# Kernel tuning notes

Hardware: AMD Instinct MI355X
Metric: run time of the kernel (lower is better)

## Reference

```python
import jax, jax.numpy as jnp
import numpy as np

# Static configuration (mirrors init_kwargs)
B, C, H, W = 4, 256, 128, 128
S, T = 512, 64          # style_dim, num style tokens
HC, HS = 4, 8           # cross-attn heads, spatial-attn heads
WS, G = 8, 4            # window size, groupnorm groups
SHARPEN = 2.0
EPS = 1e-5


def _ln(x, g, b):
    m = jnp.mean(x, -1, keepdims=True)
    v = jnp.var(x, -1, keepdims=True)
    return (x - m) * jax.lax.rsqrt(v + EPS) * g + b


def _sdpa(q, k, v, scale):
    # q,k,v: [B, nH, L, D]
    s = jnp.einsum('bhqd,bhkd->bhqk', q, k) * scale
    return jnp.einsum('bhqk,bhkd->bhqd', jax.nn.softmax(s, -1), v)


def _heads(t, nh):
    b, l, c = t.shape
    return t.reshape(b, l, nh, c // nh).transpose(0, 2, 1, 3)


def _unheads(t):
    b, nh, l, d = t.shape
    return t.transpose(0, 2, 1, 3).reshape(b, l, nh * d)


def setup_inputs() -> dict:
    key = jax.random.key(0)
    ks = iter(jax.random.split(key, 48))
    def w(shape, s=0.02):
        return jax.random.normal(next(ks), shape, jnp.float32) * s
    return {
        'x': jax.random.normal(next(ks), (B, C, H, W), jnp.float32),
        'style_code': jax.random.normal(next(ks), (B, S), jnp.float32),
        # SpatialSelfAttention params (1x1 convs == linear over channels)
        'qkv_w': w((3 * C, C)), 'spat_proj_w': w((C, C)),
        # CrossAttnAdaGN params
        'gproj_w': w((2 * C, S)),
        'gproj_b': jnp.concatenate([jnp.ones((C,), jnp.float32), jnp.zeros((C,), jnp.float32)]),
        'tokens_basis': w((T, C)),
        'sproj_w': w((C, S)), 'sproj_b': jnp.zeros((C,), jnp.float32),
        'pos_w1': w((C, 2)), 'pos_b1': jnp.zeros((C,), jnp.float32),
        'pos_w2': w((C, C)), 'pos_b2': jnp.zeros((C,), jnp.float32),
        'q_w': w((C, C)), 'q_b': jnp.zeros((C,), jnp.float32),
        'k_w': w((C, C)), 'k_b': jnp.zeros((C,), jnp.float32),
        'v_w': w((C, C)), 'v_b': jnp.zeros((C,), jnp.float32),
        'o_w': w((C, C)), 'o_b': jnp.zeros((C,), jnp.float32),
        'ffn_w1': w((2 * C, C)), 'ffn_b1': jnp.zeros((2 * C,), jnp.float32),
        'ffn_w2': w((C, 2 * C)), 'ffn_b2': jnp.zeros((C,), jnp.float32),
        'tn_g': jnp.ones((C,), jnp.float32), 'tn_b': jnp.zeros((C,), jnp.float32),
        'qn_g': jnp.ones((C,), jnp.float32), 'qn_b': jnp.zeros((C,), jnp.float32),
        'fn_g': jnp.ones((C,), jnp.float32), 'fn_b': jnp.zeros((C,), jnp.float32),
        'gamma': w((1, C, 1, 1), 0.1),
    }


def reference(x, style_code, qkv_w, spat_proj_w, gproj_w, gproj_b, tokens_basis,
              sproj_w, sproj_b, pos_w1, pos_b1, pos_w2, pos_b2,
              q_w, q_b, k_w, k_b, v_w, v_b, o_w, o_b,
              ffn_w1, ffn_b1, ffn_w2, ffn_b2,
              tn_g, tn_b, qn_g, qn_b, fn_g, fn_b, gamma):
    b = x.shape[0]
    hw = H * W
    # ---------- CrossAttnAdaGN style modulation ----------
    xg = x.reshape(b, G, C // G, H, W)
    mu = jnp.mean(xg, (2, 3, 4), keepdims=True)
    var = jnp.var(xg, (2, 3, 4), keepdims=True)
    normalized = ((xg - mu) * jax.lax.rsqrt(var + EPS)).reshape(b, C, H, W)
    gp = style_code @ gproj_w.T + gproj_b           # [B, 2C]
    scale = gp[:, :C, None, None]
    shift = gp[:, C:, None, None]
    style_tokens = tokens_basis[None] + (style_code @ sproj_w.T + sproj_b)[:, None]  # [B,T,C]
    style_tokens = _ln(style_tokens, tn_g, tn_b)
    gy = jnp.linspace(-1.0, 1.0, H)
    gx = jnp.linspace(-1.0, 1.0, W)
    grid_y, grid_x = jnp.meshgrid(gy, gx, indexing='ij')
    pos = jnp.stack([grid_x, grid_y], -1).reshape(hw, 2)                 # [HW,2]
    pos_emb = jax.nn.silu(pos @ pos_w1.T + pos_b1) @ pos_w2.T + pos_b2   # [HW,C]
    tok = normalized.transpose(0, 2, 3, 1).reshape(b, hw, C)
    q_in = _ln(tok + pos_emb[None], qn_g, qn_b)
    q = _heads(q_in @ q_w.T + q_b, HC)                 # [B,HC,HW,hd]
    k = _heads(style_tokens @ k_w.T + k_b, HC)         # [B,HC,T,hd]
    v = _heads(style_tokens @ v_w.T + v_b, HC)
    hd = C // HC
    sc = _unheads(_sdpa(q, k, v, SHARPEN / jnp.sqrt(jnp.float32(hd))))   # [B,HW,C]
    sc = sc @ o_w.T + o_b
    sc = sc + jax.nn.silu(_ln(sc, fn_g, fn_b) @ ffn_w1.T + ffn_b1) @ ffn_w2.T + ffn_b2
    sc_sp = sc.transpose(0, 2, 1).reshape(b, C, H, W)
    adagn = normalized * scale + shift + sc_sp * gamma
    h = x + adagn  # gate = 1.0, residual style modulation
    # ---------- shifted-window self-attention ----------
    sh = WS // 2
    xr = jnp.roll(h, (-sh, -sh), (2, 3))
    qkv = jnp.einsum('oi,bihw->bohw', qkv_w, xr)
    qs, ks_, vs = jnp.split(qkv, 3, axis=1)
    def win(t):  # [B,C,H,W] -> [B*nWin, WS*WS, C]
        return t.reshape(b, C, H // WS, WS, W // WS, WS).transpose(0, 2, 4, 3, 5, 1).reshape(-1, WS * WS, C)
    hd2 = C // HS
    qh = _heads(win(qs), HS)
    kh = _heads(win(ks_), HS)
    vh = _heads(win(vs), HS)
    out = _unheads(_sdpa(qh, kh, vh, 1.0 / jnp.sqrt(jnp.float32(hd2))))
    out = out.reshape(b, H // WS, W // WS, WS, WS, C).transpose(0, 5, 1, 3, 2, 4).reshape(b, C, H, W)
    out = jnp.roll(out, (sh, sh), (2, 3))
    out = jnp.einsum('oi,bihw->bohw', spat_proj_w, out)
    return h + out
```

## Files before the change

kernel.cpp:

```cpp
#include <hip/hip_runtime.h>
#include <stdint.h>

#define DEV __device__ __forceinline__

typedef unsigned short u16;
typedef unsigned int u32;
typedef __attribute__((ext_vector_type(8))) __bf16 bf16x8;
typedef __attribute__((ext_vector_type(4))) float f32x4;

DEV u16 f2b(float f) {
  u32 u = __float_as_uint(f);
  u32 r = (u + 0x7FFFu + ((u >> 16) & 1u)) >> 16;
  return (u16)r;
}
DEV float b2f(u16 u) { return __uint_as_float(((u32)u) << 16); }
DEV void up2(u32 u, float& a, float& b) {
  a = __uint_as_float(u << 16);
  b = __uint_as_float(u & 0xffff0000u);
}
DEV void up8(uint4 t, float* d) {
  up2(t.x, d[0], d[1]); up2(t.y, d[2], d[3]);
  up2(t.z, d[4], d[5]); up2(t.w, d[6], d[7]);
}
DEV float silu_f(float v) { return v / (1.0f + __expf(-v)); }

DEV float redmax16(float v) {
  v = fmaxf(v, __shfl_xor(v, 1));
  v = fmaxf(v, __shfl_xor(v, 2));
  v = fmaxf(v, __shfl_xor(v, 4));
  v = fmaxf(v, __shfl_xor(v, 8));
  return v;
}
DEV float redsum16(float v) {
  v += __shfl_xor(v, 1);
  v += __shfl_xor(v, 2);
  v += __shfl_xor(v, 4);
  v += __shfl_xor(v, 8);
  return v;
}

DEV void gload16(const u16* g, u16* l) {
  __builtin_amdgcn_global_load_lds(
      (const __attribute__((address_space(1))) uint32_t*)(g),
      (__attribute__((address_space(3))) uint32_t*)(l), 16, 0, 0);
}

struct WConv {
  const float* s0; const float* s1; const float* s2; const float* s3;
  const float* s4; const float* s5; const float* s6;
  u16* d0; u16* d1; u16* d2; u16* d3; u16* d4; u16* d5; u16* d6;
};
__global__ void k_conv_all(WConv wc) {
  int i = blockIdx.x * 256 + threadIdx.x;
  if (i >= 180224) return;
  const float* sp[7] = {wc.s0, wc.s1, wc.s2, wc.s3, wc.s4, wc.s5, wc.s6};
  u16* dp[7] = {wc.d0, wc.d1, wc.d2, wc.d3, wc.d4, wc.d5, wc.d6};
  const int n4[7] = {16384, 16384, 32768, 32768, 49152, 16384, 16384};
  int rem = i, seg = 0;
#pragma unroll
  for (int s = 0; s < 7; ++s) {
    if (rem < n4[s]) { seg = s; break; }
    rem -= n4[s];
  }
  float4 v = ((const float4*)sp[seg])[rem];
  u16 t[4] = {f2b(v.x), f2b(v.y), f2b(v.z), f2b(v.w)};
  *(uint2*)(dp[seg] + (rem << 2)) = *(uint2*)t;
}

DEV void breduce2(float& a, float& b, float* red, int tid) {
#pragma unroll
  for (int off = 32; off > 0; off >>= 1) {
    a += __shfl_down(a, off);
    b += __shfl_down(b, off);
  }
  int lane = tid & 63, wv = tid >> 6;
  if (lane == 0) { red[wv * 2] = a; red[wv * 2 + 1] = b; }
  __syncthreads();
  a = red[0] + red[2] + red[4] + red[6];
  b = red[1] + red[3] + red[5] + red[7];
}

template <int XB>
__global__ void k_gn_partial(const float* __restrict__ x, float* __restrict__ partials,
                             u16* __restrict__ xb) {
  __shared__ float red[8];
  int chunk = blockIdx.x;
  size_t base4 = ((size_t)chunk) << 12;
  const float4* x4 = (const float4*)x;
  float a = 0.f, b = 0.f;
#pragma unroll 4
  for (int i = 0; i < 16; ++i) {
    size_t idx = base4 + (i << 8) + threadIdx.x;
    float4 v = x4[idx];
    a += v.x + v.y + v.z + v.w;
    b += v.x * v.x + v.y * v.y + v.z * v.z + v.w * v.w;
    if (XB) {
      u16 t[4] = {f2b(v.x), f2b(v.y), f2b(v.z), f2b(v.w)};
      *(uint2*)(xb + (idx << 2)) = *(uint2*)t;
    }
  }
  breduce2(a, b, red, threadIdx.x);
  if (threadIdx.x == 0) { partials[chunk * 2] = a; partials[chunk * 2 + 1] = b; }
}

__global__ void k_gn_final(const float* __restrict__ partials, float* __restrict__ stats) {
  int g = blockIdx.x, lane = threadIdx.x;
  float a = partials[(((g << 6) + lane) << 1)];
  float b = partials[(((g << 6) + lane) << 1) + 1];
#pragma unroll
  for (int off = 32; off > 0; off >>= 1) {
    a += __shfl_down(a, off);
    b += __shfl_down(b, off);
  }
  if (lane == 0) {
    float mean = a * (1.f / 1048576.f);
    float var = b * (1.f / 1048576.f) - mean * mean;
    stats[g << 1] = mean;
    stats[(g << 1) + 1] = rsqrtf(var + 1e-5f);
  }
}

__global__ void k_style(const float* __restrict__ sc, const float* __restrict__ gw,
                        const float* __restrict__ gb, const float* __restrict__ sw,
                        const float* __restrict__ sb, float* __restrict__ gp,
                        float* __restrict__ stok) {
  __shared__ float row[512];
  int b = blockIdx.y, part = blockIdx.x, tid = threadIdx.x;
  row[tid] = sc[(b << 9) + tid];
  row[tid + 256] = sc[(b << 9) + tid + 256];
  __syncthreads();
  if (part < 2) {
    int o = (part << 8) + tid;
    float s = gb[o];
    const float* wr = gw + ((size_t)o << 9);
#pragma unroll 8
    for (int j = 0; j < 512; ++j) s += row[j] * wr[j];
    gp[(b << 9) + o] = s;
  } else {
    float s = sb[tid];
    const float* wr = sw + ((size_t)tid << 9);
#pragma unroll 8
    for (int j = 0; j < 512; ++j) s += row[j] * wr[j];
    stok[(b << 8) + tid] = s;
  }
}

__global__ void k_styk(const float* __restrict__ tb, const float* __restrict__ stok,
                       const float* __restrict__ g, const float* __restrict__ bt,
                       float* __restrict__ styk) {
  __shared__ float red[8];
  int r = blockIdx.x;
  int b = r >> 6, t = r & 63;
  int c = threadIdx.x;
  float v = tb[(t << 8) + c] + stok[(b << 8) + c];
  float a = v, bb = v * v;
  breduce2(a, bb, red, c);
  float mean = a * (1.f / 256.f);
  float var = bb * (1.f / 256.f) - mean * mean;
  float rs = rsqrtf(var + 1e-5f);
  styk[((size_t)r << 8) + c] = (v - mean) * rs * g[c] + bt[c];
}

__global__ void k_kv(const float* __restrict__ styk, const float* __restrict__ kw,
                     const float* __restrict__ kb, const float* __restrict__ vw,
                     const float* __restrict__ vb, u16* __restrict__ kmat,
                     u16* __restrict__ vmat) {
  __shared__ float srow[256];
  int r = blockIdx.x, c = threadIdx.x;
  srow[c] = styk[((size_t)r << 8) + c];
  __syncthreads();
  float sk = kb[c], sv = vb[c];
  const float* kr = kw + ((size_t)c << 8);
  const float* vr = vw + ((size_t)c << 8);
#pragma unroll 8
  for (int j = 0; j < 256; ++j) { sk += srow[j] * kr[j]; sv += srow[j] * vr[j]; }
  kmat[((size_t)r << 8) + c] = f2b(sk);
  vmat[((size_t)r << 8) + c] = f2b(sv);
}

__global__ void k_posh(const float* __restrict__ w1, const float* __restrict__ b1,
                       u16* __restrict__ posh) {
  int i = blockIdx.x * 256 + threadIdx.x;
  int stride = gridDim.x * 256;
  for (; i < 16384 * 256; i += stride) {
    int p = i >> 8, c = i & 255;
    int y = p >> 7, x = p & 127;
    float gx = -1.f + 2.f * (float)x / 127.f;
    float gy = -1.f + 2.f * (float)y / 127.f;
    float v = gx * w1[c << 1] + gy * w1[(c << 1) + 1] + b1[c];
    posh[i] = f2b(silu_f(v));
  }
}

template <int ACT, int BIAS, int RES, int SPLIT>
__global__ __launch_bounds__(256, 2) void k_gemm2(
    const u16* __restrict__ A, const u16* __restrict__ Bw,
    const float* __restrict__ bias, const u16* __restrict__ res,
    u16* __restrict__ o0, u16* __restrict__ o1, u16* __restrict__ o2,
    int M, int N, int K) {
  __shared__ __align__(16) u16 lds[17408];
  u16* sA = lds;
  u16* sB = lds + 4096;
  const int tid = threadIdx.x;
  const int lane = tid & 63, wv = tid >> 6;
  const int nx = gridDim.x;
  const int L = blockIdx.x + nx * blockIdx.y;
  const int xcd = L & 7;
  const int t = L >> 3;
  const int nblk = t % nx;
  const int mblk = ((t / nx) << 3) + xcd;
  const int m0 = mblk << 7, n0 = nblk << 7;
  const int l15 = lane & 15, lg = lane >> 4;
  const int wr = wv >> 1, wc = wv & 1;

  const int gofs = (((lane & 3) ^ ((lane >> 3) & 3)) << 3);
  const int lrow = lane >> 2;
  const u16* Ag0 = A + (size_t)(m0 + (wv << 5) + lrow) * K + gofs;
  const u16* Ag1 = A + (size_t)(m0 + (wv << 5) + 16 + lrow) * K + gofs;
  const u16* Bg0 = Bw + (size_t)(n0 + (wv << 5) + lrow) * K + gofs;
  const u16* Bg1 = Bw + (size_t)(n0 + (wv << 5) + 16 + lrow) * K + gofs;
  u16* lA0 = sA + (wv << 10);
  u16* lA1 = sA + (wv << 10) + 512;
  u16* lB0 = sB + (wv << 10);
  u16* lB1 = sB + (wv << 10) + 512;

  const int roff = l15 * 32 + (((lg ^ ((l15 >> 1) & 3))) << 3);
  const int abase = (wr << 6) * 32;
  const int bbase = (wc << 6) * 32;

  f32x4 acc[4][4];
  f32x4 zz = {0.f, 0.f, 0.f, 0.f};
#pragma unroll
  for (int mi = 0; mi < 4; ++mi)
#pragma unroll
    for (int ni = 0; ni < 4; ++ni) acc[mi][ni] = zz;

  for (int kt = 0; kt < K; kt += 32) {
    __syncthreads();
    gload16(Ag0 + kt, lA0);
    gload16(Ag1 + kt, lA1);
    gload16(Bg0 + kt, lB0);
    gload16(Bg1 + kt, lB1);
    __syncthreads();
    bf16x8 af[4], bfv[4];
#pragma unroll
    for (int mi = 0; mi < 4; ++mi) af[mi] = *(const bf16x8*)&sA[abase + mi * 512 + roff];
#pragma unroll
    for (int ni = 0; ni < 4; ++ni) bfv[ni] = *(const bf16x8*)&sB[bbase + ni * 512 + roff];
#pragma unroll
    for (int mi = 0; mi < 4; ++mi)
#pragma unroll
      for (int ni = 0; ni < 4; ++ni)
        acc[mi][ni] = __builtin_amdgcn_mfma_f32_16x16x32_bf16(af[mi], bfv[ni], acc[mi][ni], 0, 0, 0);
  }

  float bv[4];
#pragma unroll
  for (int ni = 0; ni < 4; ++ni)
    bv[ni] = BIAS ? bias[n0 + (wc << 6) + (ni << 4) + l15] : 0.0f;
  __syncthreads();
  const int lg4 = lg << 2;
#pragma unroll
  for (int mi = 0; mi < 4; ++mi) {
#pragma unroll
    for (int ni = 0; ni < 4; ++ni) {
#pragma unroll
      for (int r = 0; r < 4; ++r) {
        int row = (wr << 6) + (mi << 4) + lg4 + r;
        int col = (wc << 6) + (ni << 4) + l15;
        float v = acc[mi][ni][r] + bv[ni];
        if (ACT == 1) v = silu_f(v);
        lds[row * 136 + col] = f2b(v);
      }
    }
  }
  __syncthreads();
  u16* obase;
  int cb, ldc;
  if (SPLIT) {
    int sel = n0 >> 8;
    obase = sel == 0 ? o0 : (sel == 1 ? o1 : o2);
    cb = n0 & 255;
    ldc = 256;
  } else {
    obase = o0;
    cb = n0;
    ldc = N;
  }
#pragma unroll
  for (int i = 0; i < 8; ++i) {
    int flat = (i << 8) + tid;
    int row = flat >> 4, c8 = (flat & 15) << 3;
    uint4 vv = *(const uint4*)&lds[row * 136 + c8];
    size_t oi = (size_t)(m0 + row) * ldc + cb + c8;
    if (RES) {
      uint4 rr = *(const uint4*)(res + oi);
      float a8[8], r8[8];
      up8(vv, a8);
      up8(rr, r8);
      u16 t8[8];
#pragma unroll
      for (int e = 0; e < 8; ++e) t8[e] = f2b(a8[e] + r8[e]);
      vv = *(const uint4*)t8;
    }
    *(uint4*)(obase + oi) = vv;
  }
}

template <int XB>
__global__ __launch_bounds__(256) void k_tokpe2(
    const float* __restrict__ x, const u16* __restrict__ xb,
    const float* __restrict__ stats, const u16* __restrict__ pe,
    const float* __restrict__ qg, const float* __restrict__ qb2,
    u16* __restrict__ tokq) {
  __shared__ u16 T[256 * 72];
  __shared__ float red[64][8];
  const int tid = threadIdx.x;
  const int p0 = blockIdx.x << 6, b = blockIdx.y;
  {
    const int c = tid;
    const int g = (b << 2) + (c >> 6);
    const float mu = stats[g << 1], rs = stats[(g << 1) + 1];
    const size_t base = (((size_t)(b << 8) + c) << 14) + p0;
#pragma unroll
    for (int j8 = 0; j8 < 8; ++j8) {
      float f[8];
      if (XB) {
        up8(*(const uint4*)(xb + base + (j8 << 3)), f);
      } else {
        float4 v0 = *(const float4*)(x + base + (j8 << 3));
        float4 v1 = *(const float4*)(x + base + (j8 << 3) + 4);
        f[0] = v0.x; f[1] = v0.y; f[2] = v0.z; f[3] = v0.w;
        f[4] = v1.x; f[5] = v1.y; f[6] = v1.z; f[7] = v1.w;
      }
      u16 t8[8];
#pragma unroll
      for (int e = 0; e < 8; ++e) t8[e] = f2b((f[e] - mu) * rs);
      *(uint4*)&T[c * 72 + (j8 << 3)] = *(uint4*)t8;
    }
  }
  __syncthreads();
  const int p = tid & 63, cq = tid >> 6;
  const size_t pebase = (((size_t)(p0 + p)) << 8) + (cq << 6);
  float vbuf[64];
  float a = 0.f, s = 0.f;
#pragma unroll
  for (int q = 0; q < 8; ++q) {
    float pf[8];
    up8(*(const uint4*)(pe + pebase + (q << 3)), pf);
#pragma unroll
    for (int e = 0; e < 8; ++e) {
      int j = (q << 3) + e;
      float v = b2f(T[((cq << 6) + j) * 72 + p]) + pf[e];
      vbuf[j] = v;
      a += v; s += v * v;
    }
  }
  red[p][cq << 1] = a;
  red[p][(cq << 1) + 1] = s;
  __syncthreads();
  float sa = red[p][0] + red[p][2] + red[p][4] + red[p][6];
  float ss = red[p][1] + red[p][3] + red[p][5] + red[p][7];
  float mean = sa * (1.f / 256.f);
  float var = ss * (1.f / 256.f) - mean * mean;
  float rsg = rsqrtf(var + 1e-5f);
  const size_t orow = (((size_t)(b << 14) + p0 + p) << 8) + (cq << 6);
#pragma unroll
  for (int q = 0; q < 8; ++q) {
    u16 t8[8];
#pragma unroll
    for (int e = 0; e < 8; ++e) {
      int j = (q << 3) + e;
      t8[e] = f2b((vbuf[j] - mean) * rsg * qg[(cq << 6) + j] + qb2[(cq << 6) + j]);
    }
    *(uint4*)(tokq + orow + (q << 3)) = *(uint4*)t8;
  }
}

__global__ __launch_bounds__(256) void k_rowln8(const u16* __restrict__ in,
                                                const float* __restrict__ g,
                                                const float* __restrict__ bt,
                                                u16* __restrict__ out) {
  __shared__ float gs[256], bs[256];
  int tid = threadIdx.x;
  gs[tid] = g[tid];
  bs[tid] = bt[tid];
  __syncthreads();
  size_t base = (((size_t)(blockIdx.x << 5) + (tid >> 3)) << 8) + ((tid & 7) << 5);
  float v[32];
#pragma unroll
  for (int q = 0; q < 4; ++q) up8(*(const uint4*)(in + base + (q << 3)), &v[q << 3]);
  float a = 0.f, b = 0.f;
#pragma unroll
  for (int j = 0; j < 32; ++j) { a += v[j]; b += v[j] * v[j]; }
#pragma unroll
  for (int m = 1; m <= 4; m <<= 1) { a += __shfl_xor(a, m); b += __shfl_xor(b, m); }
  float mean = a * (1.f / 256.f);
  float var = b * (1.f / 256.f) - mean * mean;
  float rs = rsqrtf(var + 1e-5f);
  int c0 = (tid & 7) << 5;
#pragma unroll
  for (int q = 0; q < 4; ++q) {
    u16 tmp[8];
#pragma unroll
    for (int e = 0; e < 8; ++e) {
      int j = (q << 3) + e;
      tmp[e] = f2b((v[j] - mean) * rs * gs[c0 + j] + bs[c0 + j]);
    }
    *(uint4*)(out + base + (q << 3)) = *(uint4*)tmp;
  }
}

__global__ __launch_bounds__(256, 2) void k_cross_mfma(
    const u16* __restrict__ qmat, const u16* __restrict__ kmat,
    const u16* __restrict__ vmat, u16* __restrict__ attn_out) {
  __shared__ u16 Kl[64 * 72];
  __shared__ u16 Vt[64 * 72];
  __shared__ u16 Pl[4][64 * 72];
  const int tid = threadIdx.x;
  const int lane = tid & 63, wv = tid >> 6;
  const int l15 = lane & 15, lg = lane >> 4;
  const int b = blockIdx.z, h = blockIdx.y;
  const int q0 = blockIdx.x << 8;
  for (int c = tid; c < 512; c += 256) {
    int t = c >> 3, dg = (c & 7) << 3;
    size_t src = (((size_t)(b << 6) + t) << 8) + (h << 6) + dg;
    *(uint4*)&Kl[t * 72 + dg] = *(const uint4*)(kmat + src);
    uint4 vv = *(const uint4*)(vmat + src);
    const u16* pv = (const u16*)&vv;
#pragma unroll
    for (int e = 0; e < 8; ++e) Vt[(dg + e) * 72 + t] = pv[e];
  }
  __syncthreads();
  const size_t qrow0 = (size_t)(b << 14) + q0 + (wv << 6);
  f32x4 acc[4][4];
  f32x4 zz = {0.f, 0.f, 0.f, 0.f};
#pragma unroll
  for (int mi = 0; mi < 4; ++mi)
#pragma unroll
    for (int ni = 0; ni < 4; ++ni) acc[mi][ni] = zz;
#pragma unroll
  for (int ks = 0; ks < 2; ++ks) {
    bf16x8 a[4], bbf[4];
#pragma unroll
    for (int mi = 0; mi < 4; ++mi)
      a[mi] = *(const bf16x8*)(qmat + ((qrow0 + (mi << 4) + l15) << 8) + (h << 6) +
                               (ks << 5) + (lg << 3));
#pragma unroll
    for (int ni = 0; ni < 4; ++ni)
      bbf[ni] = *(const bf16x8*)&Kl[((ni << 4) + l15) * 72 + (ks << 5) + (lg << 3)];
#pragma unroll
    for (int mi = 0; mi < 4; ++mi)
#pragma unroll
      for (int ni = 0; ni < 4; ++ni)
        acc[mi][ni] = __builtin_amdgcn_mfma_f32_16x16x32_bf16(a[mi], bbf[ni], acc[mi][ni], 0, 0, 0);
  }
  const float SC = 0.25f;
#pragma unroll
  for (int mi = 0; mi < 4; ++mi) {
#pragma unroll
    for (int r = 0; r < 4; ++r) {
      float rm = acc[mi][0][r];
#pragma unroll
      for (int ni = 1; ni < 4; ++ni) rm = fmaxf(rm, acc[mi][ni][r]);
      rm = redmax16(rm);
      float pv[4];
      float rs = 0.f;
#pragma unroll
      for (int ni = 0; ni < 4; ++ni) {
        pv[ni] = __expf((acc[mi][ni][r] - rm) * SC);
        rs += pv[ni];
      }
      rs = redsum16(rs);
      float inv = 1.f / rs;
      int row = (mi << 4) + (lg << 2) + r;
#pragma unroll
      for (int ni = 0; ni < 4; ++ni)
        Pl[wv][row * 72 + (ni << 4) + l15] = f2b(pv[ni] * inv);
    }
  }
  __syncthreads();
  f32x4 o[4][4];
#pragma unroll
  for (int mi = 0; mi < 4; ++mi)
#pragma unroll
    for (int ni = 0; ni < 4; ++ni) o[mi][ni] = zz;
#pragma unroll
  for (int ks = 0; ks < 2; ++ks) {
    bf16x8 a[4], bbf[4];
#pragma unroll
    for (int mi = 0; mi < 4; ++mi)
      a[mi] = *(const bf16x8*)&Pl[wv][((mi << 4) + l15) * 72 + (ks << 5) + (lg << 3)];
#pragma unroll
    for (int ni = 0; ni < 4; ++ni)
      bbf[ni] = *(const bf16x8*)&Vt[((ni << 4) + l15) * 72 + (ks << 5) + (lg << 3)];
#pragma unroll
    for (int mi = 0; mi < 4; ++mi)
#pragma unroll
      for (int ni = 0; ni < 4; ++ni)
        o[mi][ni] = __builtin_amdgcn_mfma_f32_16x16x32_bf16(a[mi], bbf[ni], o[mi][ni], 0, 0, 0);
  }
  __syncthreads();
#pragma unroll
  for (int mi = 0; mi < 4; ++mi)
#pragma unroll
    for (int ni = 0; ni < 4; ++ni)
#pragma unroll
      for (int r = 0; r < 4; ++r)
        Pl[wv][((mi << 4) + (lg << 2) + r) * 72 + (ni << 4) + l15] = f2b(o[mi][ni][r]);
  __syncthreads();
  const int l8r = lane >> 3, l8c = lane & 7;
#pragma unroll
  for (int it = 0; it < 8; ++it) {
    int row = (it << 3) + l8r;
    uint4 vv = *(const uint4*)&Pl[wv][row * 72 + (l8c << 3)];
    *(uint4*)(attn_out + ((qrow0 + row) << 8) + (h << 6) + (l8c << 3)) = vv;
  }
}

__global__ __launch_bounds__(256, 2) void k_win_mfma(
    const u16* __restrict__ qb, const u16* __restrict__ kbuf,
    const u16* __restrict__ vbuf, u16* __restrict__ wout) {
  __shared__ u16 Vt[4][32 * 72];
  __shared__ u16 Pl[4][64 * 72];
  const int tid = threadIdx.x;
  const int lane = tid & 63, wv = tid >> 6;
  const int l15 = lane & 15, lg = lane >> 4;
  const int win = blockIdx.x, b = blockIdx.y;
  const int wbase = ((win >> 4) << 10) + ((win & 15) << 3);
  const size_t bbase = (size_t)b << 14;
  const float SC = 0.17677669529663687f;
  f32x4 zz = {0.f, 0.f, 0.f, 0.f};
#pragma unroll 1
  for (int h2 = 0; h2 < 2; ++h2) {
    const int h = (wv << 1) + h2;
    const int co = h << 5;
    {
      int p = wbase + ((lane >> 3) << 7) + (lane & 7);
      const u16* src = vbuf + ((bbase + p) << 8) + co;
#pragma unroll
      for (int c = 0; c < 4; ++c) {
        uint4 vv = *(const uint4*)(src + (c << 3));
        const u16* pe = (const u16*)&vv;
#pragma unroll
        for (int e = 0; e < 8; ++e) Vt[wv][((c << 3) + e) * 72 + lane] = pe[e];
      }
    }
    f32x4 acc[4][4];
#pragma unroll
    for (int mi = 0; mi < 4; ++mi)
#pragma unroll
      for (int ni = 0; ni < 4; ++ni) acc[mi][ni] = zz;
    {
      bf16x8 a[4], bbf[4];
#pragma unroll
      for (int mi = 0; mi < 4; ++mi) {
        int t = (mi << 4) + l15;
        int p = wbase + ((t >> 3) << 7) + (t & 7);
        a[mi] = *(const bf16x8*)(qb + ((bbase + p) << 8) + co + (lg << 3));
      }
#pragma unroll
      for (int ni = 0; ni < 4; ++ni) {
        int t = (ni << 4) + l15;
        int p = wbase + ((t >> 3) << 7) + (t & 7);
        bbf[ni] = *(const bf16x8*)(kbuf + ((bbase + p) << 8) + co + (lg << 3));
      }
#pragma unroll
      for (int mi = 0; mi < 4; ++mi)
#pragma unroll
        for (int ni = 0; ni < 4; ++ni)
          acc[mi][ni] = __builtin_amdgcn_mfma_f32_16x16x32_bf16(a[mi], bbf[ni], acc[mi][ni], 0, 0, 0);
    }
#pragma unroll
    for (int mi = 0; mi < 4; ++mi) {
#pragma unroll
      for (int r = 0; r < 4; ++r) {
        float rm = acc[mi][0][r];
#pragma unroll
        for (int ni = 1; ni < 4; ++ni) rm = fmaxf(rm, acc[mi][ni][r]);
        rm = redmax16(rm);
        float pv[4];
        float rs = 0.f;
#pragma unroll
        for (int ni = 0; ni < 4; ++ni) {
          pv[ni] = __expf((acc[mi][ni][r] - rm) * SC);
          rs += pv[ni];
        }
        rs = redsum16(rs);
        float inv = 1.f / rs;
        int row = (mi << 4) + (lg << 2) + r;
#pragma unroll
        for (int ni = 0; ni < 4; ++ni)
          Pl[wv][row * 72 + (ni << 4) + l15] = f2b(pv[ni] * inv);
      }
    }
    __syncthreads();
    f32x4 o[4][2];
#pragma unroll
    for (int mi = 0; mi < 4; ++mi)
#pragma unroll
      for (int ni = 0; ni < 2; ++ni) o[mi][ni] = zz;
#pragma unroll
    for (int ks = 0; ks < 2; ++ks) {
      bf16x8 a[4], bbf[2];
#pragma unroll
      for (int mi = 0; mi < 4; ++mi)
        a[mi] = *(const bf16x8*)&Pl[wv][((mi << 4) + l15) * 72 + (ks << 5) + (lg << 3)];
#pragma unroll
      for (int ni = 0; ni < 2; ++ni)
        bbf[ni] = *(const bf16x8*)&Vt[wv][((ni << 4) + l15) * 72 + (ks << 5) + (lg << 3)];
#pragma unroll
      for (int mi = 0; mi < 4; ++mi)
#pragma unroll
        for (int ni = 0; ni < 2; ++ni)
          o[mi][ni] = __builtin_amdgcn_mfma_f32_16x16x32_bf16(a[mi], bbf[ni], o[mi][ni], 0, 0, 0);
    }
    __syncthreads();
#pragma unroll
    for (int mi = 0; mi < 4; ++mi)
#pragma unroll
      for (int ni = 0; ni < 2; ++ni)
#pragma unroll
        for (int r = 0; r < 4; ++r)
          Pl[wv][((mi << 4) + (lg << 2) + r) * 72 + (ni << 4) + l15] = f2b(o[mi][ni][r]);
    __syncthreads();
#pragma unroll
    for (int it = 0; it < 4; ++it) {
      int row = (it << 4) + (lane >> 2);
      int cg = (lane & 3) << 3;
      uint4 vv = *(const uint4*)&Pl[wv][row * 72 + cg];
      int p = wbase + ((row >> 3) << 7) + (row & 7);
      *(uint4*)(wout + ((bbase + p) << 8) + co + cg) = vv;
    }
    __syncthreads();
  }
}

template <int XB>
__global__ void k_xrt(const float* __restrict__ x, const u16* __restrict__ xb,
                      const u16* __restrict__ sc2, const float* __restrict__ stats,
                      const float* __restrict__ gp, const float* __restrict__ gamma,
                      u16* __restrict__ xrt) {
  __shared__ float A[64][33];
  __shared__ float Bt[32][65];
  int p0 = blockIdx.x << 6, c0 = blockIdx.y << 5, b = blockIdx.z;
  int tid = threadIdx.x;
#pragma unroll
  for (int i = 0; i < 8; ++i) {
    int flat = (i << 8) + tid;
    int pi = flat >> 5, ci = flat & 31;
    A[pi][ci] = b2f(sc2[(((size_t)(b << 14) + p0 + pi) << 8) + c0 + ci]);
  }
  __syncthreads();
#pragma unroll
  for (int i = 0; i < 8; ++i) {
    int flat = (i << 8) + tid;
    int cc = flat >> 6, px = flat & 63;
    int cch = c0 + cc;
    int g = (b << 2) + (cch >> 6);
    float mu = stats[g << 1], rs = stats[(g << 1) + 1];
    size_t xi = (((size_t)(b << 8) + cch) << 14) + p0 + px;
    float xv = XB ? b2f(xb[xi]) : x[xi];
    float val = xv + (xv - mu) * rs * gp[(b << 9) + cch] + gp[(b << 9) + 256 + cch] +
                A[px][cc] * gamma[cch];
    Bt[cc][px] = val;
  }
  __syncthreads();
#pragma unroll
  for (int i = 0; i < 8; ++i) {
    int flat = (i << 8) + tid;
    int xi2 = flat >> 5, ci = flat & 31;
    int p = p0 + xi2;
    int yy = p >> 7, xx = p & 127;
    int pr = (((yy + 124) & 127) << 7) + ((xx + 124) & 127);
    xrt[(((size_t)(b << 14) + pr) << 8) + c0 + ci] = f2b(Bt[ci][xi2]);
  }
}

__global__ void k_final2(const u16* __restrict__ xr, const u16* __restrict__ out2,
                         float* __restrict__ dout) {
  __shared__ float L[64][33];
  int bx = blockIdx.x;
  int y = bx >> 1, x0 = (bx & 1) << 6;
  int c0 = blockIdx.y << 5, b = blockIdx.z;
  int tid = threadIdx.x;
#pragma unroll
  for (int i = 0; i < 8; ++i) {
    int flat = (i << 8) + tid;
    int xi = flat >> 5, ci = flat & 31;
    int xx = x0 + xi;
    int pr = (((y + 124) & 127) << 7) + ((xx + 124) & 127);
    size_t ii = (((size_t)(b << 14) + pr) << 8) + c0 + ci;
    L[xi][ci] = b2f(xr[ii]) + b2f(out2[ii]);
  }
  __syncthreads();
#pragma unroll
  for (int i = 0; i < 8; ++i) {
    int flat = (i << 8) + tid;
    int cc = flat >> 6, xi2 = flat & 63;
    size_t idx = (((size_t)(b << 8) + c0 + cc) << 14) + (y << 7) + x0 + xi2;
    dout[idx] = L[xi2][cc];
  }
}

extern "C" void kernel_launch(void* const* d_in, const int* in_sizes, int n_in,
                              void* d_out, int out_size, void* d_ws, size_t ws_size,
                              hipStream_t stream) {
  (void)in_sizes; (void)n_in; (void)out_size;
  const float* x = (const float*)d_in[0];
  const float* style = (const float*)d_in[1];
  const float* qkv_w = (const float*)d_in[2];
  const float* spat_w = (const float*)d_in[3];
  const float* gproj_w = (const float*)d_in[4];
  const float* gproj_b = (const float*)d_in[5];
  const float* tokens_basis = (const float*)d_in[6];
  const float* sproj_w = (const float*)d_in[7];
  const float* sproj_b = (const float*)d_in[8];
  const float* pos_w1 = (const float*)d_in[9];
  const float* pos_b1 = (const float*)d_in[10];
  const float* pos_w2 = (const float*)d_in[11];
  const float* pos_b2 = (const float*)d_in[12];
  const float* q_w = (const float*)d_in[13];
  const float* q_b = (const float*)d_in[14];
  const float* k_w = (const float*)d_in[15];
  const float* k_b = (const float*)d_in[16];
  const float* v_w = (const float*)d_in[17];
  const float* v_b = (const float*)d_in[18];
  const float* o_w = (const float*)d_in[19];
  const float* o_b = (const float*)d_in[20];
  const float* ffn_w1 = (const float*)d_in[21];
  const float* ffn_b1 = (const float*)d_in[22];
  const float* ffn_w2 = (const float*)d_in[23];
  const float* ffn_b2 = (const float*)d_in[24];
  const float* tn_g = (const float*)d_in[25];
  const float* tn_b = (const float*)d_in[26];
  const float* qn_g = (const float*)d_in[27];
  const float* qn_b = (const float*)d_in[28];
  const float* fn_g = (const float*)d_in[29];
  const float* fn_b = (const float*)d_in[30];
  const float* gamma = (const float*)d_in[31];
  float* dout = (float*)d_out;

  char* w = (char*)d_ws;
  size_t off = 0;
  auto alloc = [&](size_t sz) {
    char* p = w + off;
    off += (sz + 255) & ~(size_t)255;
    return (void*)p;
  };
  float* partials = (float*)alloc(1024 * 2 * 4);
  float* stats = (float*)alloc(32 * 4);
  float* gp = (float*)alloc(4 * 512 * 4);
  float* stok = (float*)alloc(4 * 256 * 4);
  float* styk = (float*)alloc(4 * 64 * 256 * 4);
  u16* kmat = (u16*)alloc(4 * 64 * 256 * 2);
  u16* vmat = (u16*)alloc(4 * 64 * 256 * 2);
  u16* wb_q = (u16*)alloc(65536 * 2);
  u16* wb_o = (u16*)alloc(65536 * 2);
  u16* wb_w1 = (u16*)alloc(131072 * 2);
  u16* wb_w2 = (u16*)alloc(131072 * 2);
  u16* wb_qkv = (u16*)alloc(196608 * 2);
  u16* wb_sp = (u16*)alloc(65536 * 2);
  u16* wb_p2 = (u16*)alloc(65536 * 2);
  const size_t SLOT = (size_t)65536 * 256 * 2;
  u16* S0 = (u16*)alloc(SLOT);
  u16* S1 = (u16*)alloc(SLOT);
  u16* S2 = (u16*)alloc(SLOT);
  size_t off_base = off;
  u16* xb = (u16*)alloc((size_t)67108864 * 2);
  if (ws_size < off_base) return;
  const int XB = (ws_size >= off) ? 1 : 0;

  u16* ffn_h = (u16*)d_out;
  u16* kwin = (u16*)d_out;
  u16* vwin = (u16*)d_out + (size_t)65536 * 256;

  WConv wc = {q_w, o_w, ffn_w1, ffn_w2, qkv_w, spat_w, pos_w2,
              wb_q, wb_o, wb_w1, wb_w2, wb_qkv, wb_sp, wb_p2};
  k_conv_all<<<704, 256, 0, stream>>>(wc);

  if (XB) k_gn_partial<1><<<1024, 256, 0, stream>>>(x, partials, xb);
  else k_gn_partial<0><<<1024, 256, 0, stream>>>(x, partials, xb);
  k_gn_final<<<16, 64, 0, stream>>>(partials, stats);

  k_style<<<dim3(3, 4), 256, 0, stream>>>(style, gproj_w, gproj_b, sproj_w, sproj_b, gp, stok);
  k_styk<<<256, 256, 0, stream>>>(tokens_basis, stok, tn_g, tn_b, styk);
  k_kv<<<256, 256, 0, stream>>>(styk, k_w, k_b, v_w, v_b, kmat, vmat);

  k_posh<<<4096, 256, 0, stream>>>(pos_w1, pos_b1, S0);
  k_gemm2<0, 1, 0, 0><<<dim3(2, 128), 256, 0, stream>>>(S0, wb_p2, pos_b2, nullptr,
                                                        S1, nullptr, nullptr, 16384, 256, 256);

  if (XB) k_tokpe2<1><<<dim3(256, 4), 256, 0, stream>>>(x, xb, stats, S1, qn_g, qn_b, S2);
  else k_tokpe2<0><<<dim3(256, 4), 256, 0, stream>>>(x, xb, stats, S1, qn_g, qn_b, S2);

  k_gemm2<0, 1, 0, 0><<<dim3(2, 512), 256, 0, stream>>>(S2, wb_q, q_b, nullptr,
                                                        S1, nullptr, nullptr, 65536, 256, 256);
  k_cross_mfma<<<dim3(64, 4, 4), 256, 0, stream>>>(S1, kmat, vmat, S0);
  k_gemm2<0, 1, 0, 0><<<dim3(2, 512), 256, 0, stream>>>(S0, wb_o, o_b, nullptr,
                                                        S2, nullptr, nullptr, 65536, 256, 256);

  k_rowln8<<<2048, 256, 0, stream>>>(S2, fn_g, fn_b, S1);
  k_gemm2<1, 1, 0, 0><<<dim3(4, 512), 256, 0, stream>>>(S1, wb_w1, ffn_b1, nullptr,
                                                        ffn_h, nullptr, nullptr, 65536, 512, 256);
  k_gemm2<0, 1, 1, 0><<<dim3(2, 512), 256, 0, stream>>>(ffn_h, wb_w2, ffn_b2, S2,
                                                        S0, nullptr, nullptr, 65536, 256, 512);

  if (XB) k_xrt<1><<<dim3(256, 8, 4), 256, 0, stream>>>(x, xb, S0, stats, gp, gamma, S1);
  else k_xrt<0><<<dim3(256, 8, 4), 256, 0, stream>>>(x, xb, S0, stats, gp, gamma, S1);

  k_gemm2<0, 0, 0, 1><<<dim3(6, 512), 256, 0, stream>>>(S1, wb_qkv, nullptr, nullptr,
                                                        S2, kwin, vwin, 65536, 768, 256);

  k_win_mfma<<<dim3(256, 4), 256, 0, stream>>>(S2, kwin, vwin, S0);
  k_gemm2<0, 0, 0, 0><<<dim3(2, 512), 256, 0, stream>>>(S0, wb_sp, nullptr, nullptr,
                                                        S2, nullptr, nullptr, 65536, 256, 256);

  k_final2<<<dim3(256, 8, 4), 256, 0, stream>>>(S1, S2, dout);
}
```

Measured before the change: 420.3 us.

## Store window QKV in window-contiguous row order to simplify window attention loads

Result: no change. 426.3 us, median of 2 (+1.4%).

```diff
diff --git a/kernel.cpp b/kernel.cpp
--- a/kernel.cpp
+++ b/kernel.cpp
@@ -37,6 +37,11 @@
   v += __shfl_xor(v, 4);
   v += __shfl_xor(v, 8);
   return v;
+}
+
+DEV int wperm(int p) {
+  int y = p >> 7, x = p & 127;
+  return ((((y >> 3) << 4) + (x >> 3)) << 6) + ((y & 7) << 3) + (x & 7);
 }
 
 DEV void gload16(const u16* g, u16* l) {
@@ -292,7 +297,14 @@
     int flat = (i << 8) + tid;
     int row = flat >> 4, c8 = (flat & 15) << 3;
     uint4 vv = *(const uint4*)&lds[row * 136 + c8];
-    size_t oi = (size_t)(m0 + row) * ldc + cb + c8;
+    size_t oi;
+    if (SPLIT) {
+      int m = m0 + row;
+      int orow = (m & ~16383) | wperm(m & 16383);
+      oi = (size_t)orow * 256 + cb + c8;
+    } else {
+      oi = (size_t)(m0 + row) * ldc + cb + c8;
+    }
     if (RES) {
       uint4 rr = *(const uint4*)(res + oi);
       float a8[8], r8[8];
@@ -527,8 +539,7 @@
   const int lane = tid & 63, wv = tid >> 6;
   const int l15 = lane & 15, lg = lane >> 4;
   const int win = blockIdx.x, b = blockIdx.y;
-  const int wbase = ((win >> 4) << 10) + ((win & 15) << 3);
-  const size_t bbase = (size_t)b << 14;
+  const size_t rowbase = (size_t)(b << 14) + (win << 6);
   const float SC = 0.17677669529663687f;
   f32x4 zz = {0.f, 0.f, 0.f, 0.f};
 #pragma unroll 1
@@ -536,8 +547,7 @@
     const int h = (wv << 1) + h2;
     const int co = h << 5;
     {
-      int p = wbase + ((lane >> 3) << 7) + (lane & 7);
-      const u16* src = vbuf + ((bbase + p) << 8) + co;
+      const u16* src = vbuf + ((rowbase + lane) << 8) + co;
 #pragma unroll
       for (int c = 0; c < 4; ++c) {
         uint4 vv = *(const uint4*)(src + (c << 3));
@@ -554,17 +564,11 @@
     {
       bf16x8 a[4], bbf[4];
 #pragma unroll
-      for (int mi = 0; mi < 4; ++mi) {
-        int t = (mi << 4) + l15;
-        int p = wbase + ((t >> 3) << 7) + (t & 7);
-        a[mi] = *(const bf16x8*)(qb + ((bbase + p) << 8) + co + (lg << 3));
-      }
-#pragma unroll
-      for (int ni = 0; ni < 4; ++ni) {
-        int t = (ni << 4) + l15;
-        int p = wbase + ((t >> 3) << 7) + (t & 7);
-        bbf[ni] = *(const bf16x8*)(kbuf + ((bbase + p) << 8) + co + (lg << 3));
-      }
+      for (int mi = 0; mi < 4; ++mi)
+        a[mi] = *(const bf16x8*)(qb + ((rowbase + (mi << 4) + l15) << 8) + co + (lg << 3));
+#pragma unroll
+      for (int ni = 0; ni < 4; ++ni)
+        bbf[ni] = *(const bf16x8*)(kbuf + ((rowbase + (ni << 4) + l15) << 8) + co + (lg << 3));
 #pragma unroll
       for (int mi = 0; mi < 4; ++mi)
 #pragma unroll
@@ -629,8 +633,7 @@
       int row = (it << 4) + (lane >> 2);
       int cg = (lane & 3) << 3;
       uint4 vv = *(const uint4*)&Pl[wv][row * 72 + cg];
-      int p = wbase + ((row >> 3) << 7) + (row & 7);
-      *(uint4*)(wout + ((bbase + p) << 8) + co + cg) = vv;
+      *(uint4*)(wout + ((rowbase + row) << 8) + co + cg) = vv;
     }
     __syncthreads();
   }
@@ -691,7 +694,8 @@
     int xx = x0 + xi;
     int pr = (((y + 124) & 127) << 7) + ((xx + 124) & 127);
     size_t ii = (((size_t)(b << 14) + pr) << 8) + c0 + ci;
-    L[xi][ci] = b2f(xr[ii]) + b2f(out2[ii]);
+    size_t ii2 = (((size_t)(b << 14) + wperm(pr)) << 8) + c0 + ci;
+    L[xi][ci] = b2f(xr[ii]) + b2f(out2[ii2]);
   }
   __syncthreads();
 #pragma unroll
@@ -767,7 +771,7 @@
   u16* S1 = (u16*)alloc(SLOT);
   u16* S2 = (u16*)alloc(SLOT);
   size_t off_base = off;
-  u16* xb = (u16*)alloc((size_t)67108864 * 2);
+  u16* xb = (u16*)alloc((size_t)16777216 * 2);
   if (ws_size < off_base) return;
   const int XB = (ws_size >= off) ? 1 : 0;
 
```
